# Kernel optimization log

Measured on AMD Instinct MI355X. Metric: run time of the kernel, lower is better.

Reference implementation:

```python
import jax, jax.numpy as jnp
import numpy as np


def _conv(x, w, b, stride, pad):
    y = jax.lax.conv_general_dilated(x, w, (stride, stride), [(pad, pad), (pad, pad)],
                                     dimension_numbers=('NCHW', 'OIHW', 'NCHW'))
    return y + b[None, :, None, None]


def _maxpool(x, k, s, pad=0):
    # PyTorch MaxPool2d pads with -inf
    return jax.lax.reduce_window(x, -jnp.inf, jax.lax.max,
                                 (1, 1, k, k), (1, 1, s, s),
                                 [(0, 0), (0, 0), (pad, pad), (pad, pad)])


def _squash(s):
    # squash along last axis: ||s||^2/(1+||s||^2) * s/||s||
    sq = jnp.sum(s * s, axis=-1, keepdims=True)
    return (sq / (1.0 + sq)) * s / jnp.sqrt(sq + 1e-8)


def setup_inputs() -> dict:
    key = jax.random.key(0)
    ks = jax.random.split(key, 16)

    def w(k, shape, fan_in):
        return jax.random.normal(k, shape, jnp.float32) / np.float32(np.sqrt(fan_in))

    inp = {}
    inp['x'] = jax.random.normal(ks[0], (64, 3, 227, 227), jnp.float32)
    # AlexNet conv stack
    inp['w1'] = w(ks[1], (96, 3, 11, 11), 3 * 11 * 11);   inp['b1'] = jnp.zeros((96,), jnp.float32)
    inp['w2'] = w(ks[2], (256, 96, 5, 5), 96 * 5 * 5);    inp['b2'] = jnp.zeros((256,), jnp.float32)
    inp['w3'] = w(ks[3], (384, 256, 3, 3), 256 * 3 * 3);  inp['b3'] = jnp.zeros((384,), jnp.float32)
    inp['w4'] = w(ks[4], (384, 384, 3, 3), 384 * 3 * 3);  inp['b4'] = jnp.zeros((384,), jnp.float32)
    inp['w5'] = w(ks[5], (256, 384, 3, 3), 384 * 3 * 3);  inp['b5'] = jnp.zeros((256,), jnp.float32)
    # PrimaryCaps: 32 caps * 8 dims = 256 output channels
    inp['pc_w'] = w(ks[6], (256, 256, 3, 3), 256 * 3 * 3); inp['pc_b'] = jnp.zeros((256,), jnp.float32)
    # DenseCapsule transform weights [out_caps, in_caps, out_dim, in_dim]
    inp['caps_W'] = 0.01 * jax.random.normal(ks[7], (101, 1152, 16, 8), jnp.float32)
    # MLP head (torch Linear convention: [out, in])
    inp['fc1_w'] = w(ks[8], (4096, 101 * 16), 101 * 16);  inp['fc1_b'] = jnp.zeros((4096,), jnp.float32)
    inp['fc2_w'] = w(ks[9], (4096, 4096), 4096);          inp['fc2_b'] = jnp.zeros((4096,), jnp.float32)
    inp['fc3_w'] = w(ks[10], (101, 4096), 4096);          inp['fc3_b'] = jnp.zeros((101,), jnp.float32)
    return inp


def reference(x, w1, b1, w2, b2, w3, b3, w4, b4, w5, b5,
              pc_w, pc_b, caps_W, fc1_w, fc1_b, fc2_w, fc2_b, fc3_w, fc3_b):
    # --- AlexNet conv stack ---
    h = jax.nn.relu(_conv(x, w1, b1, 4, 0))   # [B,96,55,55]
    h = _maxpool(h, 3, 2, 0)                   # [B,96,27,27]
    h = jax.nn.relu(_conv(h, w2, b2, 1, 2))    # [B,256,27,27]
    h = _maxpool(h, 3, 2, 1)                   # [B,256,14,14]
    h = jax.nn.relu(_conv(h, w3, b3, 1, 1))
    h = jax.nn.relu(_conv(h, w4, b4, 1, 1))
    h = jax.nn.relu(_conv(h, w5, b5, 1, 1))    # [B,256,14,14]
    h = _maxpool(h, 3, 2, 0)                   # [B,256,6,6]

    # --- PrimaryCaps: conv -> reshape to capsules -> squash ---
    p = _conv(h, pc_w, pc_b, 1, 1)             # [B,256,6,6]
    B = p.shape[0]
    u = _squash(p.reshape(B, -1, 8))           # [B,1152,8]

    # --- DenseCapsule dynamic routing (3 iterations) ---
    x_hat = jnp.einsum('jiod,bid->bjio', caps_W, u)   # [B,101,1152,16]
    x_hat_det = jax.lax.stop_gradient(x_hat)
    b_logits = jnp.zeros((B, 101, 1152), x_hat.dtype)
    routings = 3
    for r in range(routings):
        c = jax.nn.softmax(b_logits, axis=1)  # coupling coeffs over out caps
        if r == routings - 1:
            v = _squash(jnp.einsum('bji,bjio->bjo', c, x_hat))
        else:
            v = _squash(jnp.einsum('bji,bjio->bjo', c, x_hat_det))
            b_logits = b_logits + jnp.einsum('bjo,bjio->bji', v, x_hat_det)

    # --- MLP head (dropout in eval mode = identity) ---
    f = v.reshape(B, -1)                       # [B,1616]
    f = jax.nn.relu(f @ fc1_w.T + fc1_b)
    f = jax.nn.relu(f @ fc2_w.T + fc2_b)
    return f @ fc3_w.T + fc3_b                 # [B,101]
```

## Files before the change

kernel.cpp:

```cpp
#include <hip/hip_runtime.h>
#include <math.h>


#define BATCH 64
#define NJ 101
#define NI 1152
#define BJ (BATCH * NJ)
#define IC 64
#define NIC (NI / IC)
#define LDW 132

static inline int ceil_div(int a, int b) { return (a + b - 1) / b; }

typedef __attribute__((ext_vector_type(8))) short short8;
typedef __attribute__((ext_vector_type(4))) float f32x4;

__device__ __forceinline__ unsigned short f2bf(float f) {
    unsigned u = __float_as_uint(f);
    u += 0x7FFFu + ((u >> 16) & 1u);
    return (unsigned short)(u >> 16);
}
__device__ __forceinline__ float bf2f(unsigned short h) {
    return __uint_as_float(((unsigned)h) << 16);
}

template<int K, int STRIDE, int PAD, int WOUT, bool RELU, int TCO>
__global__ __launch_bounds__(256, 3) void conv_mfma(
        const float* __restrict__ in, const float* __restrict__ wgt,
        const float* __restrict__ bias, float* __restrict__ out,
        int CIN, int COUT, int WIN) {
    constexpr int KK  = K * K;
    constexpr int NSP = WOUT * WOUT;
    constexpr int LDH = 40;
    constexpr int NT  = TCO / 32;
    __shared__ unsigned short Ahs[TCO * LDH], Als[TCO * LDH];
    __shared__ unsigned short Bhs[64 * LDH],  Bls[64 * LDH];

    const int Ktot  = CIN * KK;
    const int WINSQ = WIN * WIN;

    const int tid  = threadIdx.x;
    const int px0  = blockIdx.x * 64;
    const int co0  = blockIdx.y * TCO;
    const int wave = tid >> 6;
    const int lane = tid & 63;
    const int ln15 = lane & 15;
    const int kq   = lane >> 4;
    const int coH  = (wave & 1) * (TCO / 2);
    const int pxH  = (wave >> 1) * 32;

    const int bpx = tid & 63;
    int p    = px0 + bpx;
    int bimg = p / NSP;
    int sp   = p - bimg * NSP;
    int ho   = sp / WOUT;
    int wo   = sp - ho * WOUT;
    const int hi0   = ho * STRIDE - PAD;
    const int wi0   = wo * STRIDE - PAD;
    const int bBase = bimg * CIN * WINSQ;

    f32x4 acc[NT][2];
#pragma unroll
    for (int ct = 0; ct < NT; ++ct)
#pragma unroll
        for (int pt = 0; pt < 2; ++pt)
            acc[ct][pt] = (f32x4){0.f, 0.f, 0.f, 0.f};

    const int nchunks = (Ktot + 31) / 32;
    for (int c = 0; c < nchunks; ++c) {
        const int k0 = c * 32;
#pragma unroll
        for (int it = 0; it < TCO / 32; ++it) {
            int slot = tid + it * 256;
            int co = slot >> 3;
            int k4 = slot & 7;
            int k  = k0 + k4 * 4;
            float4 w4 = make_float4(0.f, 0.f, 0.f, 0.f);
            const float* wp = wgt + (size_t)(co0 + co) * Ktot + k;
            if (k + 3 < Ktot) {
                w4 = *(const float4*)wp;
            } else {
                if (k + 0 < Ktot) w4.x = wp[0];
                if (k + 1 < Ktot) w4.y = wp[1];
                if (k + 2 < Ktot) w4.z = wp[2];
                if (k + 3 < Ktot) w4.w = wp[3];
            }
            unsigned short h0 = f2bf(w4.x), h1 = f2bf(w4.y),
                           h2 = f2bf(w4.z), h3 = f2bf(w4.w);
            unsigned short l0 = f2bf(w4.x - bf2f(h0)), l1 = f2bf(w4.y - bf2f(h1)),
                           l2 = f2bf(w4.z - bf2f(h2)), l3 = f2bf(w4.w - bf2f(h3));
            *(uint2*)&Ahs[co * LDH + k4 * 4] =
                make_uint2(h0 | ((unsigned)h1 << 16), h2 | ((unsigned)h3 << 16));
            *(uint2*)&Als[co * LDH + k4 * 4] =
                make_uint2(l0 | ((unsigned)l1 << 16), l2 | ((unsigned)l3 << 16));
        }
#pragma unroll
        for (int it = 0; it < 4; ++it) {
            int kp = (tid >> 6) + it * 4;
            float f0 = 0.f, f1 = 0.f;
#pragma unroll
            for (int e = 0; e < 2; ++e) {
                int k = k0 + kp * 2 + e;
                float v = 0.f;
                if (k < Ktot) {
                    int ci = k / KK;
                    int r  = k - ci * KK;
                    int kh = r / K;
                    int kw = r - kh * K;
                    int hi = hi0 + kh;
                    int wi = wi0 + kw;
                    bool ok = true;
                    if (PAD > 0)
                        ok = ((unsigned)hi < (unsigned)WIN) &&
                             ((unsigned)wi < (unsigned)WIN);
                    if (ok) v = in[bBase + ci * WINSQ + hi * WIN + wi];
                }
                if (e == 0) f0 = v; else f1 = v;
            }
            unsigned short h0 = f2bf(f0), h1 = f2bf(f1);
            unsigned short l0 = f2bf(f0 - bf2f(h0)), l1 = f2bf(f1 - bf2f(h1));
            *(unsigned*)&Bhs[bpx * LDH + kp * 2] = h0 | ((unsigned)h1 << 16);
            *(unsigned*)&Bls[bpx * LDH + kp * 2] = l0 | ((unsigned)l1 << 16);
        }
        __syncthreads();

        short8 ahf[NT], alf[NT], bhf[2], blf[2];
#pragma unroll
        for (int ct = 0; ct < NT; ++ct) {
            int m = coH + ct * 16 + ln15;
            ahf[ct] = *(const short8*)&Ahs[m * LDH + kq * 8];
            alf[ct] = *(const short8*)&Als[m * LDH + kq * 8];
        }
#pragma unroll
        for (int pt = 0; pt < 2; ++pt) {
            int n = pxH + pt * 16 + ln15;
            bhf[pt] = *(const short8*)&Bhs[n * LDH + kq * 8];
            blf[pt] = *(const short8*)&Bls[n * LDH + kq * 8];
        }
#pragma unroll
        for (int ct = 0; ct < NT; ++ct)
#pragma unroll
            for (int pt = 0; pt < 2; ++pt) {
                acc[ct][pt] = __builtin_amdgcn_mfma_f32_16x16x32_bf16(
                    ahf[ct], bhf[pt], acc[ct][pt], 0, 0, 0);
                acc[ct][pt] = __builtin_amdgcn_mfma_f32_16x16x32_bf16(
                    ahf[ct], blf[pt], acc[ct][pt], 0, 0, 0);
                acc[ct][pt] = __builtin_amdgcn_mfma_f32_16x16x32_bf16(
                    alf[ct], bhf[pt], acc[ct][pt], 0, 0, 0);
            }
        __syncthreads();
    }

    float bv[NT][4];
#pragma unroll
    for (int ct = 0; ct < NT; ++ct)
#pragma unroll
        for (int r = 0; r < 4; ++r)
            bv[ct][r] = bias[co0 + coH + ct * 16 + kq * 4 + r];
#pragma unroll
    for (int pt = 0; pt < 2; ++pt) {
        int pg  = px0 + pxH + pt * 16 + ln15;
        int b2  = pg / NSP;
        int sp2 = pg - b2 * NSP;
#pragma unroll
        for (int ct = 0; ct < NT; ++ct) {
#pragma unroll
            for (int r = 0; r < 4; ++r) {
                int co = co0 + coH + ct * 16 + kq * 4 + r;
                float vv = acc[ct][pt][r] + bv[ct][r];
                if (RELU) vv = fmaxf(vv, 0.f);
                out[(size_t)(b2 * COUT + co) * NSP + sp2] = vv;
            }
        }
    }
}

template<bool RELU>
__global__ __launch_bounds__(256, 4) void fc_gemm(
        const float* __restrict__ in, const float* __restrict__ w,
        const float* __restrict__ bias, float* __restrict__ out,
        int M, int N, int Kd) {
    constexpr int KC  = 32;
    constexpr int LDA = 68;
    __shared__ float Ash[KC * LDA];
    __shared__ float Bsh[KC * LDA];

    const int tid = threadIdx.x;
    const int n0 = blockIdx.x * 64;

    const int tn = tid & 15;
    const int tm = tid >> 4;

    float acc[4][4] = {{0.f}};

    for (int k0 = 0; k0 < Kd; k0 += KC) {
#pragma unroll
        for (int it = 0; it < 2; ++it) {
            int idx = tid + it * 256;
            int n   = idx >> 3;
            int k4  = idx & 7;
            int k   = k0 + k4 * 4;
            float4 w4 = make_float4(0.f, 0.f, 0.f, 0.f);
            int ng = n0 + n;
            if (ng < N) {
                const float* wp = w + (size_t)ng * Kd + k;
                if (k + 3 < Kd) {
                    w4 = *(const float4*)wp;
                } else {
                    if (k + 0 < Kd) w4.x = wp[0];
                    if (k + 1 < Kd) w4.y = wp[1];
                    if (k + 2 < Kd) w4.z = wp[2];
                    if (k + 3 < Kd) w4.w = wp[3];
                }
            }
            Ash[(k4 * 4 + 0) * LDA + n] = w4.x;
            Ash[(k4 * 4 + 1) * LDA + n] = w4.y;
            Ash[(k4 * 4 + 2) * LDA + n] = w4.z;
            Ash[(k4 * 4 + 3) * LDA + n] = w4.w;
        }
#pragma unroll
        for (int it = 0; it < 2; ++it) {
            int idx = tid + it * 256;
            int m   = idx >> 3;
            int k4  = idx & 7;
            int k   = k0 + k4 * 4;
            float4 x4 = make_float4(0.f, 0.f, 0.f, 0.f);
            if (m < M) {
                const float* xp = in + (size_t)m * Kd + k;
                if (k + 3 < Kd) {
                    x4 = *(const float4*)xp;
                } else {
                    if (k + 0 < Kd) x4.x = xp[0];
                    if (k + 1 < Kd) x4.y = xp[1];
                    if (k + 2 < Kd) x4.z = xp[2];
                    if (k + 3 < Kd) x4.w = xp[3];
                }
            }
            Bsh[(k4 * 4 + 0) * LDA + m] = x4.x;
            Bsh[(k4 * 4 + 1) * LDA + m] = x4.y;
            Bsh[(k4 * 4 + 2) * LDA + m] = x4.z;
            Bsh[(k4 * 4 + 3) * LDA + m] = x4.w;
        }
        __syncthreads();
#pragma unroll
        for (int kk = 0; kk < KC; ++kk) {
            float4 a4 = *(const float4*)&Ash[kk * LDA + tn * 4];
            float4 b4 = *(const float4*)&Bsh[kk * LDA + tm * 4];
            float av[4] = {a4.x, a4.y, a4.z, a4.w};
            float bv[4] = {b4.x, b4.y, b4.z, b4.w};
#pragma unroll
            for (int i = 0; i < 4; ++i)
#pragma unroll
                for (int j = 0; j < 4; ++j)
                    acc[i][j] = fmaf(av[i], bv[j], acc[i][j]);
        }
        __syncthreads();
    }

#pragma unroll
    for (int i = 0; i < 4; ++i) {
        int ng = n0 + tn * 4 + i;
        if (ng >= N) continue;
        float bs = bias[ng];
#pragma unroll
        for (int j = 0; j < 4; ++j) {
            int m = tm * 4 + j;
            if (m >= M) continue;
            float vv = acc[i][j] + bs;
            if (RELU) vv = fmaxf(vv, 0.f);
            out[(size_t)m * N + ng] = vv;
        }
    }
}

__global__ void maxpool_k(const float* __restrict__ in, float* __restrict__ out,
                          int BC, int HIN, int WIN, int HOUT, int WOUT,
                          int KS, int S, int P) {
    int idx = blockIdx.x * blockDim.x + threadIdx.x;
    int total = BC * HOUT * WOUT;
    if (idx >= total) return;
    int wo = idx % WOUT;
    int ho = (idx / WOUT) % HOUT;
    int bc = idx / (WOUT * HOUT);
    int h0 = ho * S - P, w0 = wo * S - P;
    int h1 = h0 + KS, w1 = w0 + KS;
    if (h0 < 0) h0 = 0;
    if (w0 < 0) w0 = 0;
    if (h1 > HIN) h1 = HIN;
    if (w1 > WIN) w1 = WIN;
    const float* base = in + (size_t)bc * HIN * WIN;
    float m = -INFINITY;
    for (int h = h0; h < h1; h++)
        for (int w = w0; w < w1; w++)
            m = fmaxf(m, base[h * WIN + w]);
    out[idx] = m;
}

__global__ void squash_u(const float* __restrict__ p, float* __restrict__ u, int ncaps) {
    int idx = blockIdx.x * blockDim.x + threadIdx.x;
    if (idx >= ncaps) return;
    const float4* pp = (const float4*)(p + (size_t)idx * 8);
    float4 a = pp[0], b = pp[1];
    float sq = a.x*a.x + a.y*a.y + a.z*a.z + a.w*a.w
             + b.x*b.x + b.y*b.y + b.z*b.z + b.w*b.w;
    float scale = (sq / (1.f + sq)) / sqrtf(sq + 1e-8f);
    float4* uu = (float4*)(u + (size_t)idx * 8);
    float4 oa, ob;
    oa.x = a.x*scale; oa.y = a.y*scale; oa.z = a.z*scale; oa.w = a.w*scale;
    ob.x = b.x*scale; ob.y = b.y*scale; ob.z = b.z*scale; ob.w = b.w*scale;
    uu[0] = oa; uu[1] = ob;
}

__global__ void softmax_j(const float* __restrict__ blog, float* __restrict__ c,
                          int Bn, int J, int I) {
    int idx = blockIdx.x * blockDim.x + threadIdx.x;
    if (idx >= Bn * I) return;
    int b = idx / I, i = idx - b * I;
    const float* base = blog + (size_t)b * J * I + i;
    float m = -INFINITY;
    for (int j = 0; j < J; j++) m = fmaxf(m, base[(size_t)j * I]);
    float* cb = c + (size_t)b * J * I + i;
    float sum = 0.f;
    for (int j = 0; j < J; j++) {
        float e = expf(base[(size_t)j * I] - m);
        sum += e;
        cb[(size_t)j * I] = e;
    }
    float inv = 1.f / sum;
    for (int j = 0; j < J; j++) cb[(size_t)j * I] *= inv;
}

__device__ __forceinline__ void stage_W(const float* __restrict__ W,
                                        float* __restrict__ wsh,
                                        int j, int i0, int tid) {
    const float4* Wp = (const float4*)(W + ((size_t)j * NI + i0) * 128);
#pragma unroll
    for (int p = 0; p < 8; ++p) {
        int vi  = p * 256 + tid;
        int row = vi >> 5;
        int c4  = vi & 31;
        float4 f = Wp[vi];
        *(float4*)&wsh[row * LDW + c4 * 4] = f;
    }
}

__global__ __launch_bounds__(256) void route_s_w(
        const float* __restrict__ c, const float* __restrict__ u,
        const float* __restrict__ W, float* __restrict__ ppart, int uniform) {
    __shared__ float wsh[IC * LDW];
    const int tid = threadIdx.x;
    const int icb = blockIdx.x;
    const int j   = blockIdx.y;
    const int i0  = icb * IC;

    stage_W(W, wsh, j, i0, tid);
    __syncthreads();

    const int bg = tid >> 4;
    const int iq = tid & 15;
    const float invJ = 1.f / (float)NJ;

    float s[4][16];
#pragma unroll
    for (int bb = 0; bb < 4; ++bb)
#pragma unroll
        for (int o = 0; o < 16; ++o) s[bb][o] = 0.f;

#pragma unroll
    for (int k = 0; k < 4; ++k) {
        int il = iq + 16 * k;
        int ig = i0 + il;
        const float* wr = &wsh[il * LDW];
        float4 ua[4], ub[4];
        float cc[4];
#pragma unroll
        for (int bb = 0; bb < 4; ++bb) {
            int b = bg * 4 + bb;
            const float4* up = (const float4*)(u + ((size_t)b * NI + ig) * 8);
            ua[bb] = up[0];
            ub[bb] = up[1];
            cc[bb] = uniform ? invJ : c[((size_t)b * NJ + j) * NI + ig];
        }
#pragma unroll
        for (int o = 0; o < 16; ++o) {
            float4 w0 = *(const float4*)&wr[o * 8];
            float4 w1 = *(const float4*)&wr[o * 8 + 4];
#pragma unroll
            for (int bb = 0; bb < 4; ++bb) {
                float dot = w0.x*ua[bb].x + w0.y*ua[bb].y + w0.z*ua[bb].z + w0.w*ua[bb].w
                          + w1.x*ub[bb].x + w1.y*ub[bb].y + w1.z*ub[bb].z + w1.w*ub[bb].w;
                s[bb][o] = fmaf(cc[bb], dot, s[bb][o]);
            }
        }
    }

#pragma unroll
    for (int off = 8; off > 0; off >>= 1)
#pragma unroll
        for (int bb = 0; bb < 4; ++bb)
#pragma unroll
            for (int o = 0; o < 16; ++o)
                s[bb][o] += __shfl_down(s[bb][o], off, 16);

    if (iq == 0) {
#pragma unroll
        for (int bb = 0; bb < 4; ++bb) {
            int b = bg * 4 + bb;
            size_t base = ((size_t)icb * BJ + (size_t)b * NJ + j) * 16;
#pragma unroll
            for (int o4 = 0; o4 < 4; ++o4)
                *(float4*)&ppart[base + o4 * 4] =
                    make_float4(s[bb][o4*4+0], s[bb][o4*4+1], s[bb][o4*4+2], s[bb][o4*4+3]);
        }
    }
}

__global__ __launch_bounds__(64) void reduce_squash(
        const float* __restrict__ ppart, float* __restrict__ v) {
    int l = threadIdx.x >> 4;
    int o = threadIdx.x & 15;
    int bj = blockIdx.x * 4 + l;
    float s = 0.f;
    for (int ic = 0; ic < NIC; ic++)
        s += ppart[((size_t)ic * BJ + bj) * 16 + o];
    __shared__ float sarr[4][16];
    sarr[l][o] = s;
    __syncthreads();
    float ssq = 0.f;
#pragma unroll
    for (int k = 0; k < 16; k++) { float t = sarr[l][k]; ssq += t * t; }
    float scale = (ssq / (1.f + ssq)) / sqrtf(ssq + 1e-8f);
    v[(size_t)bj * 16 + o] = s * scale;
}

__global__ __launch_bounds__(256) void route_bupd_w(
        const float* __restrict__ u, const float* __restrict__ W,
        const float* __restrict__ v, float* __restrict__ blog, int accumulate) {
    __shared__ float wsh[IC * LDW];
    const int tid = threadIdx.x;
    const int icb = blockIdx.x;
    const int j   = blockIdx.y;
    const int i0  = icb * IC;

    stage_W(W, wsh, j, i0, tid);
    __syncthreads();

    const int bg = tid >> 4;
    const int iq = tid & 15;

    float vv[4][16];
#pragma unroll
    for (int bb = 0; bb < 4; ++bb) {
        int b = bg * 4 + bb;
        const float4* vp = (const float4*)(v + ((size_t)b * NJ + j) * 16);
#pragma unroll
        for (int o4 = 0; o4 < 4; ++o4) {
            float4 f = vp[o4];
            vv[bb][o4*4+0] = f.x; vv[bb][o4*4+1] = f.y;
            vv[bb][o4*4+2] = f.z; vv[bb][o4*4+3] = f.w;
        }
    }

#pragma unroll
    for (int k = 0; k < 4; ++k) {
        int il = iq + 16 * k;
        int ig = i0 + il;
        const float* wr = &wsh[il * LDW];
        float4 ua[4], ub[4];
#pragma unroll
        for (int bb = 0; bb < 4; ++bb) {
            int b = bg * 4 + bb;
            const float4* up = (const float4*)(u + ((size_t)b * NI + ig) * 8);
            ua[bb] = up[0];
            ub[bb] = up[1];
        }
        float acc[4] = {0.f, 0.f, 0.f, 0.f};
#pragma unroll
        for (int o = 0; o < 16; ++o) {
            float4 w0 = *(const float4*)&wr[o * 8];
            float4 w1 = *(const float4*)&wr[o * 8 + 4];
#pragma unroll
            for (int bb = 0; bb < 4; ++bb) {
                float dot = w0.x*ua[bb].x + w0.y*ua[bb].y + w0.z*ua[bb].z + w0.w*ua[bb].w
                          + w1.x*ub[bb].x + w1.y*ub[bb].y + w1.z*ub[bb].z + w1.w*ub[bb].w;
                acc[bb] = fmaf(vv[bb][o], dot, acc[bb]);
            }
        }
#pragma unroll
        for (int bb = 0; bb < 4; ++bb) {
            int b = bg * 4 + bb;
            size_t idx = ((size_t)b * NJ + j) * NI + ig;
            blog[idx] = accumulate ? (blog[idx] + acc[bb]) : acc[bb];
        }
    }
}

extern "C" void kernel_launch(void* const* d_in, const int* in_sizes, int n_in,
                              void* d_out, int out_size, void* d_ws, size_t ws_size,
                              hipStream_t stream) {
    const float* x     = (const float*)d_in[0];
    const float* w1    = (const float*)d_in[1];
    const float* b1    = (const float*)d_in[2];
    const float* w2    = (const float*)d_in[3];
    const float* b2    = (const float*)d_in[4];
    const float* w3    = (const float*)d_in[5];
    const float* b3    = (const float*)d_in[6];
    const float* w4    = (const float*)d_in[7];
    const float* b4    = (const float*)d_in[8];
    const float* w5    = (const float*)d_in[9];
    const float* b5    = (const float*)d_in[10];
    const float* pc_w  = (const float*)d_in[11];
    const float* pc_b  = (const float*)d_in[12];
    const float* capsW = (const float*)d_in[13];
    const float* fc1_w = (const float*)d_in[14];
    const float* fc1_b = (const float*)d_in[15];
    const float* fc2_w = (const float*)d_in[16];
    const float* fc2_b = (const float*)d_in[17];
    const float* fc3_w = (const float*)d_in[18];
    const float* fc3_b = (const float*)d_in[19];
    float* outp = (float*)d_out;

    char* ws = (char*)d_ws;
    float* A  = (float*)ws;
    float* Bb = (float*)(ws + ((size_t)80 << 20));
    float* Dd = (float*)(ws + ((size_t)100 << 20));
    float* blog  = A;
    float* csm   = A + 7446528;
    float* ppart = A + 2 * 7446528;
    float* vcap = Dd;
    float* f1   = Dd + 131072;
    float* f2   = Dd + 131072 + 262144;

    const int B = BATCH;

    conv_mfma<11, 4, 0, 55, true, 96><<<dim3(3025, 1), dim3(256), 0, stream>>>(
        x, w1, b1, A, 3, 96, 227);
    maxpool_k<<<dim3(ceil_div(B * 96 * 27 * 27, 256)), dim3(256), 0, stream>>>(
        A, Bb, B * 96, 55, 55, 27, 27, 3, 2, 0);
    conv_mfma<5, 1, 2, 27, true, 128><<<dim3(729, 2), dim3(256), 0, stream>>>(
        Bb, w2, b2, A, 96, 256, 27);
    maxpool_k<<<dim3(ceil_div(B * 256 * 14 * 14, 256)), dim3(256), 0, stream>>>(
        A, Bb, B * 256, 27, 27, 14, 14, 3, 2, 1);
    conv_mfma<3, 1, 1, 14, true, 128><<<dim3(196, 3), dim3(256), 0, stream>>>(
        Bb, w3, b3, A, 256, 384, 14);
    conv_mfma<3, 1, 1, 14, true, 128><<<dim3(196, 3), dim3(256), 0, stream>>>(
        A, w4, b4, Bb, 384, 384, 14);
    conv_mfma<3, 1, 1, 14, true, 128><<<dim3(196, 2), dim3(256), 0, stream>>>(
        Bb, w5, b5, A, 384, 256, 14);
    maxpool_k<<<dim3(ceil_div(B * 256 * 6 * 6, 256)), dim3(256), 0, stream>>>(
        A, Bb, B * 256, 14, 14, 6, 6, 3, 2, 0);
    conv_mfma<3, 1, 1, 6, false, 64><<<dim3(36, 4), dim3(256), 0, stream>>>(
        Bb, pc_w, pc_b, A, 256, 256, 6);
    squash_u<<<dim3(ceil_div(B * 1152, 256)), dim3(256), 0, stream>>>(A, Bb, B * 1152);

    dim3 rgrid(NIC, NJ);
    route_s_w<<<rgrid, dim3(256), 0, stream>>>(csm, Bb, capsW, ppart, 1);
    reduce_squash<<<dim3(BJ / 4), dim3(64), 0, stream>>>(ppart, vcap);
    route_bupd_w<<<rgrid, dim3(256), 0, stream>>>(Bb, capsW, vcap, blog, 0);
    softmax_j<<<dim3(ceil_div(B * NI, 256)), dim3(256), 0, stream>>>(
        blog, csm, B, NJ, NI);
    route_s_w<<<rgrid, dim3(256), 0, stream>>>(csm, Bb, capsW, ppart, 0);
    reduce_squash<<<dim3(BJ / 4), dim3(64), 0, stream>>>(ppart, vcap);
    route_bupd_w<<<rgrid, dim3(256), 0, stream>>>(Bb, capsW, vcap, blog, 1);
    softmax_j<<<dim3(ceil_div(B * NI, 256)), dim3(256), 0, stream>>>(
        blog, csm, B, NJ, NI);
    route_s_w<<<rgrid, dim3(256), 0, stream>>>(csm, Bb, capsW, ppart, 0);
    reduce_squash<<<dim3(BJ / 4), dim3(64), 0, stream>>>(ppart, vcap);

    fc_gemm<true><<<dim3(64), dim3(256), 0, stream>>>(vcap, fc1_w, fc1_b, f1, B, 4096, 1616);
    fc_gemm<true><<<dim3(64), dim3(256), 0, stream>>>(f1, fc2_w, fc2_b, f2, B, 4096, 4096);
    fc_gemm<false><<<dim3(2), dim3(256), 0, stream>>>(f2, fc3_w, fc3_b, outp, B, 101, 4096);
}
```

Measured before the change: 3.918 ms.

## Pre-split conv weights and pack activations as hi/lo bf16 pairs

Adds a split_w pre-pass that converts each conv weight tensor once into hi/lo bf16 arrays, so conv blocks load ready-made bf16 pairs instead of redoing the split per tile. Maxpool and the middle conv layers now write activations as packed hi/lo bf16 words, so later convs skip the per-element split when building B tiles. Launch bounds go from 3 to 4 blocks per CU. This costs extra workspace, six small pre-pass launches per call, and depends on the workspace being large enough; otherwise the old float path is used.

```diff
diff --git a/kernel.cpp b/kernel.cpp
--- a/kernel.cpp
+++ b/kernel.cpp
@@ -23,12 +23,30 @@
 __device__ __forceinline__ float bf2f(unsigned short h) {
     return __uint_as_float(((unsigned)h) << 16);
 }
-
-template<int K, int STRIDE, int PAD, int WOUT, bool RELU, int TCO>
-__global__ __launch_bounds__(256, 3) void conv_mfma(
-        const float* __restrict__ in, const float* __restrict__ wgt,
-        const float* __restrict__ bias, float* __restrict__ out,
-        int CIN, int COUT, int WIN) {
+__device__ __forceinline__ unsigned packsplit(float v) {
+    unsigned short h = f2bf(v);
+    unsigned short l = f2bf(v - bf2f(h));
+    return ((unsigned)h << 16) | l;
+}
+
+__global__ void split_w(const float* __restrict__ w, unsigned short* __restrict__ hi,
+                        unsigned short* __restrict__ lo, int Ktot, int Kp, int total) {
+    int idx = blockIdx.x * 256 + threadIdx.x;
+    if (idx >= total) return;
+    int co = idx / Kp, kp = idx - co * Kp;
+    float v = (kp < Ktot) ? w[(size_t)co * Ktot + kp] : 0.f;
+    unsigned short h = f2bf(v);
+    hi[idx] = h;
+    lo[idx] = f2bf(v - bf2f(h));
+}
+
+template<int K, int STRIDE, int PAD, int WOUT, bool RELU, int TCO,
+         bool INPK, bool OUTPK>
+__global__ __launch_bounds__(256, 4) void conv_mfma(
+        const void* __restrict__ inv, const float* __restrict__ wgt,
+        const unsigned short* __restrict__ whi, const unsigned short* __restrict__ wlo,
+        const float* __restrict__ bias, void* __restrict__ outv,
+        int CIN, int COUT, int WIN, int Kp) {
     constexpr int KK  = K * K;
     constexpr int NSP = WOUT * WOUT;
     constexpr int LDH = 40;
@@ -59,6 +77,9 @@
     const int wi0   = wo * STRIDE - PAD;
     const int bBase = bimg * CIN * WINSQ;
 
+    const int aco = tid >> 3;
+    const int ak4 = tid & 7;
+
     f32x4 acc[NT][2];
 #pragma unroll
     for (int ct = 0; ct < NT; ++ct)
@@ -69,58 +90,99 @@
     const int nchunks = (Ktot + 31) / 32;
     for (int c = 0; c < nchunks; ++c) {
         const int k0 = c * 32;
-#pragma unroll
-        for (int it = 0; it < TCO / 32; ++it) {
-            int slot = tid + it * 256;
-            int co = slot >> 3;
-            int k4 = slot & 7;
-            int k  = k0 + k4 * 4;
-            float4 w4 = make_float4(0.f, 0.f, 0.f, 0.f);
-            const float* wp = wgt + (size_t)(co0 + co) * Ktot + k;
-            if (k + 3 < Ktot) {
-                w4 = *(const float4*)wp;
-            } else {
-                if (k + 0 < Ktot) w4.x = wp[0];
-                if (k + 1 < Ktot) w4.y = wp[1];
-                if (k + 2 < Ktot) w4.z = wp[2];
-                if (k + 3 < Ktot) w4.w = wp[3];
-            }
-            unsigned short h0 = f2bf(w4.x), h1 = f2bf(w4.y),
-                           h2 = f2bf(w4.z), h3 = f2bf(w4.w);
-            unsigned short l0 = f2bf(w4.x - bf2f(h0)), l1 = f2bf(w4.y - bf2f(h1)),
-                           l2 = f2bf(w4.z - bf2f(h2)), l3 = f2bf(w4.w - bf2f(h3));
-            *(uint2*)&Ahs[co * LDH + k4 * 4] =
-                make_uint2(h0 | ((unsigned)h1 << 16), h2 | ((unsigned)h3 << 16));
-            *(uint2*)&Als[co * LDH + k4 * 4] =
-                make_uint2(l0 | ((unsigned)l1 << 16), l2 | ((unsigned)l3 << 16));
+        if (whi) {
+#pragma unroll
+            for (int it = 0; it < TCO / 32; ++it) {
+                int slot = tid + it * 256;
+                int co = slot >> 3;
+                int k4 = slot & 7;
+                int row = (co0 + co) * Kp + k0 + k4 * 4;
+                ushort4 h4 = *(const ushort4*)&whi[row];
+                ushort4 l4 = *(const ushort4*)&wlo[row];
+                *(ushort4*)&Ahs[co * LDH + k4 * 4] = h4;
+                *(ushort4*)&Als[co * LDH + k4 * 4] = l4;
+            }
+        } else {
+#pragma unroll
+            for (int it = 0; it < TCO / 32; ++it) {
+                int slot = tid + it * 256;
+                int co = slot >> 3;
+                int k4 = slot & 7;
+                int k  = k0 + k4 * 4;
+                float4 w4 = make_float4(0.f, 0.f, 0.f, 0.f);
+                const float* wp = wgt + (size_t)(co0 + co) * Ktot + k;
+                if (k + 3 < Ktot) {
+                    w4 = *(const float4*)wp;
+                } else {
+                    if (k + 0 < Ktot) w4.x = wp[0];
+                    if (k + 1 < Ktot) w4.y = wp[1];
+                    if (k + 2 < Ktot) w4.z = wp[2];
+                    if (k + 3 < Ktot) w4.w = wp[3];
+                }
+                unsigned short h0 = f2bf(w4.x), h1 = f2bf(w4.y),
+                               h2 = f2bf(w4.z), h3 = f2bf(w4.w);
+                unsigned short l0 = f2bf(w4.x - bf2f(h0)), l1 = f2bf(w4.y - bf2f(h1)),
+                               l2 = f2bf(w4.z - bf2f(h2)), l3 = f2bf(w4.w - bf2f(h3));
+                *(uint2*)&Ahs[co * LDH + k4 * 4] =
+                    make_uint2(h0 | ((unsigned)h1 << 16), h2 | ((unsigned)h3 << 16));
+                *(uint2*)&Als[co * LDH + k4 * 4] =
+                    make_uint2(l0 | ((unsigned)l1 << 16), l2 | ((unsigned)l3 << 16));
+            }
         }
 #pragma unroll
         for (int it = 0; it < 4; ++it) {
             int kp = (tid >> 6) + it * 4;
-            float f0 = 0.f, f1 = 0.f;
-#pragma unroll
-            for (int e = 0; e < 2; ++e) {
-                int k = k0 + kp * 2 + e;
-                float v = 0.f;
-                if (k < Ktot) {
-                    int ci = k / KK;
-                    int r  = k - ci * KK;
-                    int kh = r / K;
-                    int kw = r - kh * K;
-                    int hi = hi0 + kh;
-                    int wi = wi0 + kw;
-                    bool ok = true;
-                    if (PAD > 0)
-                        ok = ((unsigned)hi < (unsigned)WIN) &&
-                             ((unsigned)wi < (unsigned)WIN);
-                    if (ok) v = in[bBase + ci * WINSQ + hi * WIN + wi];
+            if (INPK) {
+                const unsigned* inp = (const unsigned*)inv;
+                unsigned u0 = 0, u1 = 0;
+#pragma unroll
+                for (int e = 0; e < 2; ++e) {
+                    int k = k0 + kp * 2 + e;
+                    unsigned v = 0;
+                    if (k < Ktot) {
+                        int ci = k / KK;
+                        int r  = k - ci * KK;
+                        int kh = r / K;
+                        int kw = r - kh * K;
+                        int hh = hi0 + kh;
+                        int ww = wi0 + kw;
+                        bool ok = true;
+                        if (PAD > 0)
+                            ok = ((unsigned)hh < (unsigned)WIN) &&
+                                 ((unsigned)ww < (unsigned)WIN);
+                        if (ok) v = inp[bBase + ci * WINSQ + hh * WIN + ww];
+                    }
+                    if (e == 0) u0 = v; else u1 = v;
                 }
-                if (e == 0) f0 = v; else f1 = v;
-            }
-            unsigned short h0 = f2bf(f0), h1 = f2bf(f1);
-            unsigned short l0 = f2bf(f0 - bf2f(h0)), l1 = f2bf(f1 - bf2f(h1));
-            *(unsigned*)&Bhs[bpx * LDH + kp * 2] = h0 | ((unsigned)h1 << 16);
-            *(unsigned*)&Bls[bpx * LDH + kp * 2] = l0 | ((unsigned)l1 << 16);
+                *(unsigned*)&Bhs[bpx * LDH + kp * 2] = (u0 >> 16) | (u1 & 0xFFFF0000u);
+                *(unsigned*)&Bls[bpx * LDH + kp * 2] = (u0 & 0xFFFFu) | (u1 << 16);
+            } else {
+                const float* inp = (const float*)inv;
+                float f0 = 0.f, f1 = 0.f;
+#pragma unroll
+                for (int e = 0; e < 2; ++e) {
+                    int k = k0 + kp * 2 + e;
+                    float v = 0.f;
+                    if (k < Ktot) {
+                        int ci = k / KK;
+                        int r  = k - ci * KK;
+                        int kh = r / K;
+                        int kw = r - kh * K;
+                        int hh = hi0 + kh;
+                        int ww = wi0 + kw;
+                        bool ok = true;
+                        if (PAD > 0)
+                            ok = ((unsigned)hh < (unsigned)WIN) &&
+                                 ((unsigned)ww < (unsigned)WIN);
+                        if (ok) v = inp[bBase + ci * WINSQ + hh * WIN + ww];
+                    }
+                    if (e == 0) f0 = v; else f1 = v;
+                }
+                unsigned short h0 = f2bf(f0), h1 = f2bf(f1);
+                unsigned short l0 = f2bf(f0 - bf2f(h0)), l1 = f2bf(f1 - bf2f(h1));
+                *(unsigned*)&Bhs[bpx * LDH + kp * 2] = h0 | ((unsigned)h1 << 16);
+                *(unsigned*)&Bls[bpx * LDH + kp * 2] = l0 | ((unsigned)l1 << 16);
+            }
         }
         __syncthreads();
 
@@ -169,8 +231,232 @@
                 int co = co0 + coH + ct * 16 + kq * 4 + r;
                 float vv = acc[ct][pt][r] + bv[ct][r];
                 if (RELU) vv = fmaxf(vv, 0.f);
-                out[(size_t)(b2 * COUT + co) * NSP + sp2] = vv;
-            }
+                size_t oi = (size_t)(b2 * COUT + co) * NSP + sp2;
+                if (OUTPK) ((unsigned*)outv)[oi] = packsplit(vv);
+                else       ((float*)outv)[oi] = vv;
+            }
+        }
+    }
+}
+
+__global__ void maxpool_pack(const float* __restrict__ in, unsigned* __restrict__ out,
+                             int BC, int HIN, int WIN, int HOUT, int WOUT,
+                             int KS, int S, int P) {
+    int idx = blockIdx.x * blockDim.x + threadIdx.x;
+    int total = BC * HOUT * WOUT;
+    if (idx >= total) return;
+    int wo = idx % WOUT;
+    int ho = (idx / WOUT) % HOUT;
+    int bc = idx / (WOUT * HOUT);
+    int h0 = ho * S - P, w0 = wo * S - P;
+    int h1 = h0 + KS, w1 = w0 + KS;
+    if (h0 < 0) h0 = 0;
+    if (w0 < 0) w0 = 0;
+    if (h1 > HIN) h1 = HIN;
+    if (w1 > WIN) w1 = WIN;
+    const float* base = in + (size_t)bc * HIN * WIN;
+    float m = -INFINITY;
+    for (int h = h0; h < h1; h++)
+        for (int w = w0; w < w1; w++)
+            m = fmaxf(m, base[h * WIN + w]);
+    out[idx] = packsplit(m);
+}
+
+__global__ void squash_u(const float* __restrict__ p, float* __restrict__ u, int ncaps) {
+    int idx = blockIdx.x * blockDim.x + threadIdx.x;
+    if (idx >= ncaps) return;
+    const float4* pp = (const float4*)(p + (size_t)idx * 8);
+    float4 a = pp[0], b = pp[1];
+    float sq = a.x*a.x + a.y*a.y + a.z*a.z + a.w*a.w
+             + b.x*b.x + b.y*b.y + b.z*b.z + b.w*b.w;
+    float scale = (sq / (1.f + sq)) / sqrtf(sq + 1e-8f);
+    float4* uu = (float4*)(u + (size_t)idx * 8);
+    float4 oa, ob;
+    oa.x = a.x*scale; oa.y = a.y*scale; oa.z = a.z*scale; oa.w = a.w*scale;
+    ob.x = b.x*scale; ob.y = b.y*scale; ob.z = b.z*scale; ob.w = b.w*scale;
+    uu[0] = oa; uu[1] = ob;
+}
+
+__global__ void softmax_j(const float* __restrict__ blog, float* __restrict__ c,
+                          int Bn, int J, int I) {
+    int idx = blockIdx.x * blockDim.x + threadIdx.x;
+    if (idx >= Bn * I) return;
+    int b = idx / I, i = idx - b * I;
+    const float* base = blog + (size_t)b * J * I + i;
+    float m = -INFINITY;
+    for (int j = 0; j < J; j++) m = fmaxf(m, base[(size_t)j * I]);
+    float* cb = c + (size_t)b * J * I + i;
+    float sum = 0.f;
+    for (int j = 0; j < J; j++) {
+        float e = expf(base[(size_t)j * I] - m);
+        sum += e;
+        cb[(size_t)j * I] = e;
+    }
+    float inv = 1.f / sum;
+    for (int j = 0; j < J; j++) cb[(size_t)j * I] *= inv;
+}
+
+__device__ __forceinline__ void stage_W(const float* __restrict__ W,
+                                        float* __restrict__ wsh,
+                                        int j, int i0, int tid) {
+    const float4* Wp = (const float4*)(W + ((size_t)j * NI + i0) * 128);
+#pragma unroll
+    for (int p = 0; p < 8; ++p) {
+        int vi  = p * 256 + tid;
+        int row = vi >> 5;
+        int c4  = vi & 31;
+        float4 f = Wp[vi];
+        *(float4*)&wsh[row * LDW + c4 * 4] = f;
+    }
+}
+
+__global__ __launch_bounds__(256) void route_s_w(
+        const float* __restrict__ c, const float* __restrict__ u,
+        const float* __restrict__ W, float* __restrict__ ppart, int uniform) {
+    __shared__ float wsh[IC * LDW];
+    const int tid = threadIdx.x;
+    const int icb = blockIdx.x;
+    const int j   = blockIdx.y;
+    const int i0  = icb * IC;
+
+    stage_W(W, wsh, j, i0, tid);
+    __syncthreads();
+
+    const int bg = tid >> 4;
+    const int iq = tid & 15;
+    const float invJ = 1.f / (float)NJ;
+
+    float s[4][16];
+#pragma unroll
+    for (int bb = 0; bb < 4; ++bb)
+#pragma unroll
+        for (int o = 0; o < 16; ++o) s[bb][o] = 0.f;
+
+#pragma unroll
+    for (int k = 0; k < 4; ++k) {
+        int il = iq + 16 * k;
+        int ig = i0 + il;
+        const float* wr = &wsh[il * LDW];
+        float4 ua[4], ub[4];
+        float cc[4];
+#pragma unroll
+        for (int bb = 0; bb < 4; ++bb) {
+            int b = bg * 4 + bb;
+            const float4* up = (const float4*)(u + ((size_t)b * NI + ig) * 8);
+            ua[bb] = up[0];
+            ub[bb] = up[1];
+            cc[bb] = uniform ? invJ : c[((size_t)b * NJ + j) * NI + ig];
+        }
+#pragma unroll
+        for (int o = 0; o < 16; ++o) {
+            float4 w0 = *(const float4*)&wr[o * 8];
+            float4 w1 = *(const float4*)&wr[o * 8 + 4];
+#pragma unroll
+            for (int bb = 0; bb < 4; ++bb) {
+                float dot = w0.x*ua[bb].x + w0.y*ua[bb].y + w0.z*ua[bb].z + w0.w*ua[bb].w
+                          + w1.x*ub[bb].x + w1.y*ub[bb].y + w1.z*ub[bb].z + w1.w*ub[bb].w;
+                s[bb][o] = fmaf(cc[bb], dot, s[bb][o]);
+            }
+        }
+    }
+
+#pragma unroll
+    for (int off = 8; off > 0; off >>= 1)
+#pragma unroll
+        for (int bb = 0; bb < 4; ++bb)
+#pragma unroll
+            for (int o = 0; o < 16; ++o)
+                s[bb][o] += __shfl_down(s[bb][o], off, 16);
+
+    if (iq == 0) {
+#pragma unroll
+        for (int bb = 0; bb < 4; ++bb) {
+            int b = bg * 4 + bb;
+            size_t base = ((size_t)icb * BJ + (size_t)b * NJ + j) * 16;
+#pragma unroll
+            for (int o4 = 0; o4 < 4; ++o4)
+                *(float4*)&ppart[base + o4 * 4] =
+                    make_float4(s[bb][o4*4+0], s[bb][o4*4+1], s[bb][o4*4+2], s[bb][o4*4+3]);
+        }
+    }
+}
+
+__global__ __launch_bounds__(64) void reduce_squash(
+        const float* __restrict__ ppart, float* __restrict__ v) {
+    int l = threadIdx.x >> 4;
+    int o = threadIdx.x & 15;
+    int bj = blockIdx.x * 4 + l;
+    float s = 0.f;
+    for (int ic = 0; ic < NIC; ic++)
+        s += ppart[((size_t)ic * BJ + bj) * 16 + o];
+    __shared__ float sarr[4][16];
+    sarr[l][o] = s;
+    __syncthreads();
+    float ssq = 0.f;
+#pragma unroll
+    for (int k = 0; k < 16; k++) { float t = sarr[l][k]; ssq += t * t; }
+    float scale = (ssq / (1.f + ssq)) / sqrtf(ssq + 1e-8f);
+    v[(size_t)bj * 16 + o] = s * scale;
+}
+
+__global__ __launch_bounds__(256) void route_bupd_w(
+        const float* __restrict__ u, const float* __restrict__ W,
+        const float* __restrict__ v, float* __restrict__ blog, int accumulate) {
+    __shared__ float wsh[IC * LDW];
+    const int tid = threadIdx.x;
+    const int icb = blockIdx.x;
+    const int j   = blockIdx.y;
+    const int i0  = icb * IC;
+
+    stage_W(W, wsh, j, i0, tid);
+    __syncthreads();
+
+    const int bg = tid >> 4;
+    const int iq = tid & 15;
+
+    float vv[4][16];
+#pragma unroll
+    for (int bb = 0; bb < 4; ++bb) {
+        int b = bg * 4 + bb;
+        const float4* vp = (const float4*)(v + ((size_t)b * NJ + j) * 16);
+#pragma unroll
+        for (int o4 = 0; o4 < 4; ++o4) {
+            float4 f = vp[o4];
+            vv[bb][o4*4+0] = f.x; vv[bb][o4*4+1] = f.y;
+            vv[bb][o4*4+2] = f.z; vv[bb][o4*4+3] = f.w;
+        }
+    }
+
+#pragma unroll
+    for (int k = 0; k < 4; ++k) {
+        int il = iq + 16 * k;
+        int ig = i0 + il;
+        const float* wr = &wsh[il * LDW];
+        float4 ua[4], ub[4];
+#pragma unroll
+        for (int bb = 0; bb < 4; ++bb) {
+            int b = bg * 4 + bb;
+            const float4* up = (const float4*)(u + ((size_t)b * NI + ig) * 8);
+            ua[bb] = up[0];
+            ub[bb] = up[1];
+        }
+        float acc[4] = {0.f, 0.f, 0.f, 0.f};
+#pragma unroll
+        for (int o = 0; o < 16; ++o) {
+            float4 w0 = *(const float4*)&wr[o * 8];
+            float4 w1 = *(const float4*)&wr[o * 8 + 4];
+#pragma unroll
+            for (int bb = 0; bb < 4; ++bb) {
+                float dot = w0.x*ua[bb].x + w0.y*ua[bb].y + w0.z*ua[bb].z + w0.w*ua[bb].w
+                          + w1.x*ub[bb].x + w1.y*ub[bb].y + w1.z*ub[bb].z + w1.w*ub[bb].w;
+                acc[bb] = fmaf(vv[bb][o], dot, acc[bb]);
+            }
+        }
+#pragma unroll
+        for (int bb = 0; bb < 4; ++bb) {
+            int b = bg * 4 + bb;
+            size_t idx = ((size_t)b * NJ + j) * NI + ig;
+            blog[idx] = accumulate ? (blog[idx] + acc[bb]) : acc[bb];
         }
     }
 }
@@ -269,228 +555,6 @@
             float vv = acc[i][j] + bs;
             if (RELU) vv = fmaxf(vv, 0.f);
             out[(size_t)m * N + ng] = vv;
-        }
-    }
-}
-
-__global__ void maxpool_k(const float* __restrict__ in, float* __restrict__ out,
-                          int BC, int HIN, int WIN, int HOUT, int WOUT,
-                          int KS, int S, int P) {
-    int idx = blockIdx.x * blockDim.x + threadIdx.x;
-    int total = BC * HOUT * WOUT;
-    if (idx >= total) return;
-    int wo = idx % WOUT;
-    int ho = (idx / WOUT) % HOUT;
-    int bc = idx / (WOUT * HOUT);
-    int h0 = ho * S - P, w0 = wo * S - P;
-    int h1 = h0 + KS, w1 = w0 + KS;
-    if (h0 < 0) h0 = 0;
-    if (w0 < 0) w0 = 0;
-    if (h1 > HIN) h1 = HIN;
-    if (w1 > WIN) w1 = WIN;
-    const float* base = in + (size_t)bc * HIN * WIN;
-    float m = -INFINITY;
-    for (int h = h0; h < h1; h++)
-        for (int w = w0; w < w1; w++)
-            m = fmaxf(m, base[h * WIN + w]);
-    out[idx] = m;
-}
-
-__global__ void squash_u(const float* __restrict__ p, float* __restrict__ u, int ncaps) {
-    int idx = blockIdx.x * blockDim.x + threadIdx.x;
-    if (idx >= ncaps) return;
-    const float4* pp = (const float4*)(p + (size_t)idx * 8);
-    float4 a = pp[0], b = pp[1];
-    float sq = a.x*a.x + a.y*a.y + a.z*a.z + a.w*a.w
-             + b.x*b.x + b.y*b.y + b.z*b.z + b.w*b.w;
-    float scale = (sq / (1.f + sq)) / sqrtf(sq + 1e-8f);
-    float4* uu = (float4*)(u + (size_t)idx * 8);
-    float4 oa, ob;
-    oa.x = a.x*scale; oa.y = a.y*scale; oa.z = a.z*scale; oa.w = a.w*scale;
-    ob.x = b.x*scale; ob.y = b.y*scale; ob.z = b.z*scale; ob.w = b.w*scale;
-    uu[0] = oa; uu[1] = ob;
-}
-
-__global__ void softmax_j(const float* __restrict__ blog, float* __restrict__ c,
-                          int Bn, int J, int I) {
-    int idx = blockIdx.x * blockDim.x + threadIdx.x;
-    if (idx >= Bn * I) return;
-    int b = idx / I, i = idx - b * I;
-    const float* base = blog + (size_t)b * J * I + i;
-    float m = -INFINITY;
-    for (int j = 0; j < J; j++) m = fmaxf(m, base[(size_t)j * I]);
-    float* cb = c + (size_t)b * J * I + i;
-    float sum = 0.f;
-    for (int j = 0; j < J; j++) {
-        float e = expf(base[(size_t)j * I] - m);
-        sum += e;
-        cb[(size_t)j * I] = e;
-    }
-    float inv = 1.f / sum;
-    for (int j = 0; j < J; j++) cb[(size_t)j * I] *= inv;
-}
-
-__device__ __forceinline__ void stage_W(const float* __restrict__ W,
-                                        float* __restrict__ wsh,
-                                        int j, int i0, int tid) {
-    const float4* Wp = (const float4*)(W + ((size_t)j * NI + i0) * 128);
-#pragma unroll
-    for (int p = 0; p < 8; ++p) {
-        int vi  = p * 256 + tid;
-        int row = vi >> 5;
-        int c4  = vi & 31;
-        float4 f = Wp[vi];
-        *(float4*)&wsh[row * LDW + c4 * 4] = f;
-    }
-}
-
-__global__ __launch_bounds__(256) void route_s_w(
-        const float* __restrict__ c, const float* __restrict__ u,
-        const float* __restrict__ W, float* __restrict__ ppart, int uniform) {
-    __shared__ float wsh[IC * LDW];
-    const int tid = threadIdx.x;
-    const int icb = blockIdx.x;
-    const int j   = blockIdx.y;
-    const int i0  = icb * IC;
-
-    stage_W(W, wsh, j, i0, tid);
-    __syncthreads();
-
-    const int bg = tid >> 4;
-    const int iq = tid & 15;
-    const float invJ = 1.f / (float)NJ;
-
-    float s[4][16];
-#pragma unroll
-    for (int bb = 0; bb < 4; ++bb)
-#pragma unroll
-        for (int o = 0; o < 16; ++o) s[bb][o] = 0.f;
-
-#pragma unroll
-    for (int k = 0; k < 4; ++k) {
-        int il = iq + 16 * k;
-        int ig = i0 + il;
-        const float* wr = &wsh[il * LDW];
-        float4 ua[4], ub[4];
-        float cc[4];
-#pragma unroll
-        for (int bb = 0; bb < 4; ++bb) {
-            int b = bg * 4 + bb;
-            const float4* up = (const float4*)(u + ((size_t)b * NI + ig) * 8);
-            ua[bb] = up[0];
-            ub[bb] = up[1];
-            cc[bb] = uniform ? invJ : c[((size_t)b * NJ + j) * NI + ig];
-        }
-#pragma unroll
-        for (int o = 0; o < 16; ++o) {
-            float4 w0 = *(const float4*)&wr[o * 8];
-            float4 w1 = *(const float4*)&wr[o * 8 + 4];
-#pragma unroll
-            for (int bb = 0; bb < 4; ++bb) {
-                float dot = w0.x*ua[bb].x + w0.y*ua[bb].y + w0.z*ua[bb].z + w0.w*ua[bb].w
-                          + w1.x*ub[bb].x + w1.y*ub[bb].y + w1.z*ub[bb].z + w1.w*ub[bb].w;
-                s[bb][o] = fmaf(cc[bb], dot, s[bb][o]);
-            }
-        }
-    }
-
-#pragma unroll
-    for (int off = 8; off > 0; off >>= 1)
-#pragma unroll
-        for (int bb = 0; bb < 4; ++bb)
-#pragma unroll
-            for (int o = 0; o < 16; ++o)
-                s[bb][o] += __shfl_down(s[bb][o], off, 16);
-
-    if (iq == 0) {
-#pragma unroll
-        for (int bb = 0; bb < 4; ++bb) {
-            int b = bg * 4 + bb;
-            size_t base = ((size_t)icb * BJ + (size_t)b * NJ + j) * 16;
-#pragma unroll
-            for (int o4 = 0; o4 < 4; ++o4)
-                *(float4*)&ppart[base + o4 * 4] =
-                    make_float4(s[bb][o4*4+0], s[bb][o4*4+1], s[bb][o4*4+2], s[bb][o4*4+3]);
-        }
-    }
-}
-
-__global__ __launch_bounds__(64) void reduce_squash(
-        const float* __restrict__ ppart, float* __restrict__ v) {
-    int l = threadIdx.x >> 4;
-    int o = threadIdx.x & 15;
-    int bj = blockIdx.x * 4 + l;
-    float s = 0.f;
-    for (int ic = 0; ic < NIC; ic++)
-        s += ppart[((size_t)ic * BJ + bj) * 16 + o];
-    __shared__ float sarr[4][16];
-    sarr[l][o] = s;
-    __syncthreads();
-    float ssq = 0.f;
-#pragma unroll
-    for (int k = 0; k < 16; k++) { float t = sarr[l][k]; ssq += t * t; }
-    float scale = (ssq / (1.f + ssq)) / sqrtf(ssq + 1e-8f);
-    v[(size_t)bj * 16 + o] = s * scale;
-}
-
-__global__ __launch_bounds__(256) void route_bupd_w(
-        const float* __restrict__ u, const float* __restrict__ W,
-        const float* __restrict__ v, float* __restrict__ blog, int accumulate) {
-    __shared__ float wsh[IC * LDW];
-    const int tid = threadIdx.x;
-    const int icb = blockIdx.x;
-    const int j   = blockIdx.y;
-    const int i0  = icb * IC;
-
-    stage_W(W, wsh, j, i0, tid);
-    __syncthreads();
-
-    const int bg = tid >> 4;
-    const int iq = tid & 15;
-
-    float vv[4][16];
-#pragma unroll
-    for (int bb = 0; bb < 4; ++bb) {
-        int b = bg * 4 + bb;
-        const float4* vp = (const float4*)(v + ((size_t)b * NJ + j) * 16);
-#pragma unroll
-        for (int o4 = 0; o4 < 4; ++o4) {
-            float4 f = vp[o4];
-            vv[bb][o4*4+0] = f.x; vv[bb][o4*4+1] = f.y;
-            vv[bb][o4*4+2] = f.z; vv[bb][o4*4+3] = f.w;
-        }
-    }
-
-#pragma unroll
-    for (int k = 0; k < 4; ++k) {
-        int il = iq + 16 * k;
-        int ig = i0 + il;
-        const float* wr = &wsh[il * LDW];
-        float4 ua[4], ub[4];
-#pragma unroll
-        for (int bb = 0; bb < 4; ++bb) {
-            int b = bg * 4 + bb;
-            const float4* up = (const float4*)(u + ((size_t)b * NI + ig) * 8);
-            ua[bb] = up[0];
-            ub[bb] = up[1];
-        }
-        float acc[4] = {0.f, 0.f, 0.f, 0.f};
-#pragma unroll
-        for (int o = 0; o < 16; ++o) {
-            float4 w0 = *(const float4*)&wr[o * 8];
-            float4 w1 = *(const float4*)&wr[o * 8 + 4];
-#pragma unroll
-            for (int bb = 0; bb < 4; ++bb) {
-                float dot = w0.x*ua[bb].x + w0.y*ua[bb].y + w0.z*ua[bb].z + w0.w*ua[bb].w
-                          + w1.x*ub[bb].x + w1.y*ub[bb].y + w1.z*ub[bb].z + w1.w*ub[bb].w;
-                acc[bb] = fmaf(vv[bb][o], dot, acc[bb]);
-            }
-        }
-#pragma unroll
-        for (int bb = 0; bb < 4; ++bb) {
-            int b = bg * 4 + bb;
-            size_t idx = ((size_t)b * NJ + j) * NI + ig;
-            blog[idx] = accumulate ? (blog[idx] + acc[bb]) : acc[bb];
         }
     }
 }
@@ -531,26 +595,65 @@
     float* f1   = Dd + 131072;
     float* f2   = Dd + 131072 + 262144;
 
+    const size_t WPL_ELEMS = 2ull * (96*384 + 256*2400 + 384*2304 +
+                                     384*3456 + 256*3456 + 256*2304);
+    const size_t WPL_NEED  = ((size_t)104 << 20) + WPL_ELEMS * 2;
+    const bool wsplit = ws_size >= WPL_NEED;
+    unsigned short* wp = (unsigned short*)(ws + ((size_t)104 << 20));
+    unsigned short *w1h=nullptr,*w1l=nullptr,*w2h=nullptr,*w2l=nullptr,
+                   *w3h=nullptr,*w3l=nullptr,*w4h=nullptr,*w4l=nullptr,
+                   *w5h=nullptr,*w5l=nullptr,*pch=nullptr,*pcl=nullptr;
+    if (wsplit) {
+        size_t off = 0;
+        auto alloc2 = [&](size_t n, unsigned short** h, unsigned short** l) {
+            *h = wp + off; *l = wp + off + n; off += 2 * n;
+        };
+        alloc2((size_t)96*384,  &w1h, &w1l);
+        alloc2((size_t)256*2400, &w2h, &w2l);
+        alloc2((size_t)384*2304, &w3h, &w3l);
+        alloc2((size_t)384*3456, &w4h, &w4l);
+        alloc2((size_t)256*3456, &w5h, &w5l);
+        alloc2((size_t)256*2304, &pch, &pcl);
+        split_w<<<dim3(ceil_div(96*384, 256)), dim3(256), 0, stream>>>(
+            w1, w1h, w1l, 363, 384, 96*384);
+        split_w<<<dim3(ceil_div(256*2400, 256)), dim3(256), 0, stream>>>(
+            w2, w2h, w2l, 2400, 2400, 256*2400);
+        split_w<<<dim3(ceil_div(384*2304, 256)), dim3(256), 0, stream>>>(
+            w3, w3h, w3l, 2304, 2304, 384*2304);
+        split_w<<<dim3(ceil_div(384*3456, 256)), dim3(256), 0, stream>>>(
+            w4, w4h, w4l, 3456, 3456, 384*3456);
+        split_w<<<dim3(ceil_div(256*3456, 256)), dim3(256), 0, stream>>>(
+            w5, w5h, w5l, 3456, 3456, 256*3456);
+        split_w<<<dim3(ceil_div(256*2304, 256)), dim3(256), 0, stream>>>(
+            pc_w, pch, pcl, 2304, 2304, 256*2304);
+    }
+
     const int B = BATCH;
 
-    conv_mfma<11, 4, 0, 55, true, 96><<<dim3(3025, 1), dim3(256), 0, stream>>>(
-        x, w1, b1, A, 3, 96, 227);
-    maxpool_k<<<dim3(ceil_div(B * 96 * 27 * 27, 256)), dim3(256), 0, stream>>>(
-        A, Bb, B * 96, 55, 55, 27, 27, 3, 2, 0);
-    conv_mfma<5, 1, 2, 27, true, 128><<<dim3(729, 2), dim3(256), 0, stream>>>(
-        Bb, w2, b2, A, 96, 256, 27);
-    maxpool_k<<<dim3(ceil_div(B * 256 * 14 * 14, 256)), dim3(256), 0, stream>>>(
-        A, Bb, B * 256, 27, 27, 14, 14, 3, 2, 1);
-    conv_mfma<3, 1, 1, 14, true, 128><<<dim3(196, 3), dim3(256), 0, stream>>>(
-        Bb, w3, b3, A, 256, 384, 14);
-    conv_mfma<3, 1, 1, 14, true, 128><<<dim3(196, 3), dim3(256), 0, stream>>>(
-        A, w4, b4, Bb, 384, 384, 14);
-    conv_mfma<3, 1, 1, 14, true, 128><<<dim3(196, 2), dim3(256), 0, stream>>>(
-        Bb, w5, b5, A, 384, 256, 14);
-    maxpool_k<<<dim3(ceil_div(B * 256 * 6 * 6, 256)), dim3(256), 0, stream>>>(
-        A, Bb, B * 256, 14, 14, 6, 6, 3, 2, 0);
-    conv_mfma<3, 1, 1, 6, false, 64><<<dim3(36, 4), dim3(256), 0, stream>>>(
-        Bb, pc_w, pc_b, A, 256, 256, 6);
+    conv_mfma<11, 4, 0, 55, true, 96, false, false>
+        <<<dim3(3025, 1), dim3(256), 0, stream>>>(
+        x, w1, w1h, w1l, b1, A, 3, 96, 227, 384);
+    maxpool_pack<<<dim3(ceil_div(B * 96 * 27 * 27, 256)), dim3(256), 0, stream>>>(
+        A, (unsigned*)Bb, B * 96, 55, 55, 27, 27, 3, 2, 0);
+    conv_mfma<5, 1, 2, 27, true, 128, true, false>
+        <<<dim3(729, 2), dim3(256), 0, stream>>>(
+        Bb, w2, w2h, w2l, b2, A, 96, 256, 27, 2400);
+    maxpool_pack<<<dim3(ceil_div(B * 256 * 14 * 14, 256)), dim3(256), 0, stream>>>(
+        A, (unsigned*)Bb, B * 256, 27, 27, 14, 14, 3, 2, 1);
+    conv_mfma<3, 1, 1, 14, true, 128, true, true>
+        <<<dim3(196, 3), dim3(256), 0, stream>>>(
+        Bb, w3, w3h, w3l, b3, A, 256, 384, 14, 2304);
+    conv_mfma<3, 1, 1, 14, true, 128, true, true>
+        <<<dim3(196, 3), dim3(256), 0, stream>>>(
+        A, w4, w4h, w4l, b4, Bb, 384, 384, 14, 3456);
+    conv_mfma<3, 1, 1, 14, true, 128, true, false>
+        <<<dim3(196, 2), dim3(256), 0, stream>>>(
+        Bb, w5, w5h, w5l, b5, A, 384, 256, 14, 3456);
+    maxpool_pack<<<dim3(ceil_div(B * 256 * 6 * 6, 256)), dim3(256), 0, stream>>>(
+        A, (unsigned*)Bb, B * 256, 14, 14, 6, 6, 3, 2, 0);
+    conv_mfma<3, 1, 1, 6, false, 64, true, false>
+        <<<dim3(36, 4), dim3(256), 0, stream>>>(
+        Bb, pc_w, pch, pcl, pc_b, A, 256, 256, 6, 2304);
     squash_u<<<dim3(ceil_div(B * 1152, 256)), dim3(256), 0, stream>>>(A, Bb, B * 1152);
 
     dim3 rgrid(NIC, NJ);
```

Result: faster. 3.485 ms (-11.1%).
